# Kernel optimization log

Measured on AMD Instinct MI355X. Metric: run time of the kernel, lower is better.

The kernel has to match this reference:

```python
import jax, jax.numpy as jnp
import numpy as np
import math

BATCH, SEQ, HIDDEN, HEADS = 2, 2048, 1024, 16
HEAD_SIZE = HIDDEN // HEADS
NEG_INF = -10000.0  # faithful to the torch module's masking constant


def setup_inputs() -> dict:
    key = jax.random.key(0)
    k1, k2, k3, k4 = jax.random.split(key, 4)
    x = jax.random.normal(k1, (BATCH, SEQ, HIDDEN), dtype=jnp.float32)
    pos_table = jax.random.normal(k2, (SEQ, HIDDEN), dtype=jnp.float32) * 0.02
    # torch nn.Linear weight layout: [out_features, in_features]
    Wqkv = jax.random.normal(k3, (3 * HIDDEN, HIDDEN), dtype=jnp.float32) * (1.0 / math.sqrt(HIDDEN))
    Wout = jax.random.normal(k4, (HIDDEN, HIDDEN), dtype=jnp.float32) * (1.0 / math.sqrt(HIDDEN))
    return {"x": x, "pos_table": pos_table, "Wqkv": Wqkv, "Wout": Wout}


def reference(x, pos_table, Wqkv, Wout):
    b, n, h = x.shape
    # positional embedding added for Q/K projection only (V uses raw x)
    xp = x + pos_table[None, :n, :]
    qk = jnp.einsum('bnd,ed->bne', xp, Wqkv[: 2 * HIDDEN])          # [b, n, 2h]
    q, k = jnp.split(qk, 2, axis=-1)
    v = jnp.einsum('bnd,ed->bne', x, Wqkv[2 * HIDDEN:])             # [b, n, h]

    def to_heads(t):  # b n (h l) -> b h n l
        return t.reshape(b, n, HEADS, HEAD_SIZE).transpose(0, 2, 1, 3)

    q, k, v = to_heads(q), to_heads(k), to_heads(v)

    scores = jnp.einsum('bhql,bhkl->bhqk', q, k) / math.sqrt(HEAD_SIZE)
    q_ind = jnp.arange(n)[:, None]
    k_ind = jnp.arange(n)[None, :]
    mask = q_ind < k_ind                                            # True where future
    scores = jnp.where(mask, NEG_INF, scores)
    probs = jax.nn.softmax(scores, axis=-1)
    combined_v = jnp.einsum('bhqk,bhkl->bhql', probs, v)            # [b, h, n, l]
    combined_v = combined_v.transpose(0, 2, 1, 3).reshape(b, n, h)  # b h q l -> b q (h l)
    out = jnp.einsum('bnd,ed->bne', combined_v, Wout)
    return out
```

## Files before the change

### kernel.cpp

```cpp
#include <hip/hip_runtime.h>
#include <hip/hip_bf16.h>
#include <stdint.h>

#define BATCH 2
#define SEQ   2048
#define HID   1024
#define NHEAD 16
#define HD    64
#define MROWS (BATCH*SEQ)

typedef __attribute__((ext_vector_type(8))) short bf16x8;
typedef __attribute__((ext_vector_type(4))) float f32x4;

__device__ inline unsigned pk2(float a, float b){
  __hip_bfloat162 h = __float22bfloat162_rn(make_float2(a, b));
  union { __hip_bfloat162 h; unsigned u; } v; v.h = h;
  return v.u;
}
__device__ inline float fexp2(float x){
#if __has_builtin(__builtin_amdgcn_exp2f)
  return __builtin_amdgcn_exp2f(x);
#else
  return exp2f(x);
#endif
}
__device__ inline void lds_load16(const short* g, short* l){
  __builtin_amdgcn_global_load_lds(
      (const __attribute__((address_space(1))) void*)g,
      (__attribute__((address_space(3))) void*)l, 16, 0, 0);
}

__global__ __launch_bounds__(256) void cast_xpos(
    const float* __restrict__ x, const float* __restrict__ pos,
    short* __restrict__ xb, short* __restrict__ xv){
  int i = blockIdx.x * 256 + threadIdx.x;
  float4 xa = ((const float4*)x)[i];
  float4 pa = ((const float4*)pos)[i & (SEQ*HID/4 - 1)];
  uint2 sb, sv;
  sb.x = pk2(xa.x + pa.x, xa.y + pa.y);
  sb.y = pk2(xa.z + pa.z, xa.w + pa.w);
  sv.x = pk2(xa.x, xa.y);
  sv.y = pk2(xa.z, xa.w);
  ((uint2*)xb)[i] = sb;
  ((uint2*)xv)[i] = sv;
}

__global__ __launch_bounds__(256) void cast_w2(
    const float* __restrict__ w1, const float* __restrict__ w2,
    short* __restrict__ o1, short* __restrict__ o2){
  int i = blockIdx.x * 256 + threadIdx.x;
  const int n1 = 3*HID*HID/4;
  const float4* src; uint2* dst; int j;
  if (i < n1){ src = (const float4*)w1; dst = (uint2*)o1; j = i; }
  else       { src = (const float4*)w2; dst = (uint2*)o2; j = i - n1; }
  float4 a = src[j];
  uint2 s;
  s.x = pk2(a.x, a.y);
  s.y = pk2(a.z, a.w);
  dst[j] = s;
}

template<bool F32OUT>
__global__ __launch_bounds__(256) void gemm_bt(
    const short* __restrict__ A0, const short* __restrict__ A1, int split_bx,
    const short* __restrict__ W, void* __restrict__ Cout, int K, int ldc,
    int qsb, float qscale){
  __shared__ alignas(16) short As[2][128*32];
  __shared__ alignas(16) short Bs[2][128*32];
  const int bx = blockIdx.x, by = blockIdx.y;
  const short* A = (bx < split_bx) ? A0 : A1;
  const int tid  = threadIdx.x;
  const int w    = tid >> 6, lane = tid & 63;
  const int g    = lane >> 4, c = lane & 15;
  const int wr   = w >> 1, wc = w & 1;

  f32x4 acc[4][4];
#pragma unroll
  for (int m = 0; m < 4; ++m)
#pragma unroll
    for (int n = 0; n < 4; ++n) acc[m][n] = (f32x4){0.f, 0.f, 0.f, 0.f};

  const short* Abase = A + (size_t)(by*128) * K;
  const short* Wbase = W + (size_t)(bx*128) * K;

  auto stage = [&](int buf, int kt){
#pragma unroll
    for (int j = 0; j < 2; ++j){
      int ci  = w*128 + j*64 + lane;
      int row = ci >> 2, sub = ci & 3;
      lds_load16(Abase + (size_t)row*K + kt + sub*8, &As[buf][(w*128 + j*64)*8]);
      lds_load16(Wbase + (size_t)row*K + kt + sub*8, &Bs[buf][(w*128 + j*64)*8]);
    }
  };

  const int nk = K >> 5;
  stage(0, 0);
  int buf = 0;
  for (int ki = 0; ki < nk; ++ki){
    __syncthreads();
    if (ki + 1 < nk) stage(buf ^ 1, (ki + 1) * 32);

    bf16x8 af[4], bfr[4];
#pragma unroll
    for (int m = 0; m < 4; ++m)
      af[m] = *(const bf16x8*)&As[buf][(wr*64 + m*16 + c)*32 + g*8];
#pragma unroll
    for (int n = 0; n < 4; ++n)
      bfr[n] = *(const bf16x8*)&Bs[buf][(wc*64 + n*16 + c)*32 + g*8];
    __builtin_amdgcn_s_setprio(1);
#pragma unroll
    for (int m = 0; m < 4; ++m)
#pragma unroll
      for (int n = 0; n < 4; ++n)
        acc[m][n] = __builtin_amdgcn_mfma_f32_16x16x32_bf16(af[m], bfr[n], acc[m][n], 0, 0, 0);
    __builtin_amdgcn_s_setprio(0);
    buf ^= 1;
  }

  const float sc = (bx < qsb) ? qscale : 1.0f;
  const int row0 = by*128 + wr*64;
  const int col0 = bx*128 + wc*64;
#pragma unroll
  for (int m = 0; m < 4; ++m)
#pragma unroll
    for (int n = 0; n < 4; ++n){
      size_t base = (size_t)(row0 + m*16 + g*4) * ldc + (col0 + n*16 + c);
      if constexpr (F32OUT){
#pragma unroll
        for (int r = 0; r < 4; ++r)
          ((float*)Cout)[base + (size_t)r*ldc] = acc[m][n][r] * sc;
      } else {
        short* p = (short*)Cout + base;
        unsigned u01 = pk2(acc[m][n][0]*sc, acc[m][n][1]*sc);
        unsigned u23 = pk2(acc[m][n][2]*sc, acc[m][n][3]*sc);
        p[0]             = (short)(u01 & 0xffff);
        p[(size_t)ldc]   = (short)(u01 >> 16);
        p[2*(size_t)ldc] = (short)(u23 & 0xffff);
        p[3*(size_t)ldc] = (short)(u23 >> 16);
      }
    }
}

__global__ __launch_bounds__(256) void attn_fwd(
    const short* __restrict__ qkv, short* __restrict__ out){
  const int bid = blockIdx.x;
  const int qt  = 31 - (bid >> 5);
  const int bh  = bid & 31;
  const int b   = bh >> 4, h = bh & 15;
  const int tid = threadIdx.x;
  const int w   = tid >> 6, lane = tid & 63;
  const int g   = lane >> 4, c = lane & 15;

  __shared__ alignas(16) short Ks[2][64*64];
  __shared__ alignas(16) short Vt[2][64*64];

  const int q0 = qt*64 + w*16;
  const size_t rowb = (size_t)b * SEQ;

  const short* qptr = qkv + (rowb + q0 + c)*3072 + h*HD;
  bf16x8 qf0 = *(const bf16x8*)(qptr + g*8);
  bf16x8 qf1 = *(const bf16x8*)(qptr + 32 + g*8);

  const short* kbase = qkv + rowb*3072 + HID   + h*HD;
  const short* vbase = qkv + rowb*3072 + 2*HID + h*HD;

  const int slot   = ((lane >> 5) << 5) | (((lane >> 2) & 3) << 3)
                   | (((lane >> 4) & 1) << 2) | (lane & 3);
  const int vchunk = slot >> 3, vcol = slot & 7;

  auto stageK = [&](int buf, int c0){
#pragma unroll
    for (int j = 0; j < 2; ++j){
      int pc  = w*128 + j*64 + lane;
      int row = pc >> 3;
      int lc  = (pc & 7) ^ (row & 7);
      lds_load16(kbase + (size_t)(c0 + row)*3072 + lc*8, &Ks[buf][(w*128 + j*64)*8]);
    }
  };
  auto loadV = [&](int c0, bf16x8& v0, bf16x8& v1){
    const short* vp = vbase + (size_t)(c0 + lane)*3072 + w*16;
    v0 = *(const bf16x8*)(vp);
    v1 = *(const bf16x8*)(vp + 8);
  };
  auto scatterV = [&](int buf, const bf16x8& v0, const bf16x8& v1){
#pragma unroll
    for (int j = 0; j < 8; ++j)
      Vt[buf][(w*16 + j)*64 + ((vchunk ^ (j & 7)) << 3) + vcol] = v0[j];
#pragma unroll
    for (int j = 0; j < 8; ++j)
      Vt[buf][(w*16 + 8 + j)*64 + ((vchunk ^ ((8 + j) & 7)) << 3) + vcol] = v1[j];
  };

  f32x4 ot[4];
#pragma unroll
  for (int dt = 0; dt < 4; ++dt) ot[dt] = (f32x4){0.f, 0.f, 0.f, 0.f};
  float mrow = -1e30f, lrow = 0.f;
  const int qg = q0 + c;

  {
    bf16x8 v0, v1;
    stageK(0, 0);
    loadV(0, v0, v1);
    scatterV(0, v0, v1);
  }
  int cur = 0;
  for (int ch = 0; ch <= qt; ++ch){
    const int c0 = ch * 64;
    __syncthreads();

    bf16x8 nv0, nv1;
    if (ch < qt){
      stageK(cur ^ 1, c0 + 64);
      loadV(c0 + 64, nv0, nv1);
    }

    f32x4 s[4];
    __builtin_amdgcn_s_setprio(1);
#pragma unroll
    for (int kt = 0; kt < 4; ++kt){
      int row = kt*16 + c;
      bf16x8 k0 = *(const bf16x8*)&Ks[cur][row*64 + ((g       ^ (row&7))<<3)];
      bf16x8 k1 = *(const bf16x8*)&Ks[cur][row*64 + (((4 + g) ^ (row&7))<<3)];
      f32x4 z = (f32x4){0.f, 0.f, 0.f, 0.f};
      s[kt] = __builtin_amdgcn_mfma_f32_16x16x32_bf16(k0, qf0, z, 0, 0, 0);
      s[kt] = __builtin_amdgcn_mfma_f32_16x16x32_bf16(k1, qf1, s[kt], 0, 0, 0);
    }
    __builtin_amdgcn_s_setprio(0);

    float pv[16];
#pragma unroll
    for (int kt = 0; kt < 4; ++kt)
#pragma unroll
      for (int r = 0; r < 4; ++r) pv[kt*4 + r] = s[kt][r];

    if (ch == qt){
#pragma unroll
      for (int kt = 0; kt < 4; ++kt)
#pragma unroll
        for (int r = 0; r < 4; ++r){
          int ki = c0 + kt*16 + g*4 + r;
          if (ki > qg) pv[kt*4 + r] = -1e30f;
        }
    }

    float a0 = fmaxf(fmaxf(pv[0],  pv[1]),  pv[2]);
    float a1 = fmaxf(fmaxf(pv[3],  pv[4]),  pv[5]);
    float a2 = fmaxf(fmaxf(pv[6],  pv[7]),  pv[8]);
    float a3 = fmaxf(fmaxf(pv[9],  pv[10]), pv[11]);
    float a4 = fmaxf(fmaxf(pv[12], pv[13]), pv[14]);
    float cm = fmaxf(fmaxf(fmaxf(a0, a1), a2), fmaxf(fmaxf(a3, a4), pv[15]));
    cm = fmaxf(cm, __shfl_xor(cm, 16));
    cm = fmaxf(cm, __shfl_xor(cm, 32));
    if (__any(cm > mrow + 8.0f)){
      float mnew  = fmaxf(mrow, cm);
      float alpha = fexp2(mrow - mnew);
      lrow *= alpha;
#pragma unroll
      for (int dt = 0; dt < 4; ++dt)
#pragma unroll
        for (int r = 0; r < 4; ++r) ot[dt][r] *= alpha;
      mrow = mnew;
    }
    float ps = 0.f;
#pragma unroll
    for (int i = 0; i < 16; ++i){ pv[i] = fexp2(pv[i] - mrow); ps += pv[i]; }
    ps += __shfl_xor(ps, 16);
    ps += __shfl_xor(ps, 32);
    lrow += ps;

    union { unsigned u[4]; bf16x8 v; } pb0, pb1;
    pb0.u[0] = pk2(pv[0],  pv[1]);  pb0.u[1] = pk2(pv[2],  pv[3]);
    pb0.u[2] = pk2(pv[4],  pv[5]);  pb0.u[3] = pk2(pv[6],  pv[7]);
    pb1.u[0] = pk2(pv[8],  pv[9]);  pb1.u[1] = pk2(pv[10], pv[11]);
    pb1.u[2] = pk2(pv[12], pv[13]); pb1.u[3] = pk2(pv[14], pv[15]);

    __builtin_amdgcn_s_setprio(1);
#pragma unroll
    for (int dt = 0; dt < 4; ++dt){
      int d = dt*16 + c;
      bf16x8 va0 = *(const bf16x8*)&Vt[cur][d*64 + ((g       ^ (d&7))<<3)];
      bf16x8 va1 = *(const bf16x8*)&Vt[cur][d*64 + (((4 + g) ^ (d&7))<<3)];
      ot[dt] = __builtin_amdgcn_mfma_f32_16x16x32_bf16(va0, pb0.v, ot[dt], 0, 0, 0);
      ot[dt] = __builtin_amdgcn_mfma_f32_16x16x32_bf16(va1, pb1.v, ot[dt], 0, 0, 0);
    }
    __builtin_amdgcn_s_setprio(0);

    if (ch < qt) scatterV(cur ^ 1, nv0, nv1);
    cur ^= 1;
  }

  float inv = 1.f / lrow;
  short* obase = out + (rowb + q0 + c)*HID + h*HD + g*4;
#pragma unroll
  for (int dt = 0; dt < 4; ++dt){
    uint2 uu;
    uu.x = pk2(ot[dt][0]*inv, ot[dt][1]*inv);
    uu.y = pk2(ot[dt][2]*inv, ot[dt][3]*inv);
    *(uint2*)(obase + dt*16) = uu;
  }
}

extern "C" void kernel_launch(void* const* d_in, const int* in_sizes, int n_in,
                              void* d_out, int out_size, void* d_ws, size_t ws_size,
                              hipStream_t stream){
  const float* x    = (const float*)d_in[0];
  const float* pos  = (const float*)d_in[1];
  const float* Wqkv = (const float*)d_in[2];
  const float* Wout = (const float*)d_in[3];

  short* xb     = (short*)d_ws;
  short* xv     = xb    + (size_t)MROWS*HID;
  short* wqkvb  = xv    + (size_t)MROWS*HID;
  short* woutb  = wqkvb + (size_t)3*HID*HID;
  short* qkv    = woutb + (size_t)HID*HID;
  short* attn_o = xb;

  cast_xpos<<<dim3(MROWS*HID/1024), 256, 0, stream>>>(x, pos, xb, xv);
  cast_w2<<<dim3(4*HID*HID/1024), 256, 0, stream>>>(Wqkv, Wout, wqkvb, woutb);

  gemm_bt<false><<<dim3(24, 32), 256, 0, stream>>>(xb, xv, 16, wqkvb, qkv, HID, 3*HID,
                                                   8, 0.18033688011112042f);

  attn_fwd<<<dim3(1024), 256, 0, stream>>>(qkv, attn_o);

  gemm_bt<true><<<dim3(8, 32), 256, 0, stream>>>(attn_o, attn_o, 8, woutb, d_out, HID, HID,
                                                 0, 1.0f);
}
```

Baseline: 197.1 us.

## Process 128 query rows per attention block to double K/V tile reuse

Each attention block now handles a 128-row query tile, with every wave owning two 16-row query groups (A and B) that share each staged K/V chunk from LDS. This halves the K/V global loads and LDS staging per query and halves the grid to 512 blocks. Waves skip chunks that lie entirely beyond their causal range. The cost is twice the accumulator and softmax registers per wave, which may lower occupancy. Causal work is also less balanced, since waves in the same block idle on the last chunks and there are fewer blocks to spread over the CUs.

```diff
diff --git a/kernel.cpp b/kernel.cpp
--- a/kernel.cpp
+++ b/kernel.cpp
@@ -144,7 +144,7 @@
 __global__ __launch_bounds__(256) void attn_fwd(
     const short* __restrict__ qkv, short* __restrict__ out){
   const int bid = blockIdx.x;
-  const int qt  = 31 - (bid >> 5);
+  const int qt  = 15 - (bid >> 5);
   const int bh  = bid & 31;
   const int b   = bh >> 4, h = bh & 15;
   const int tid = threadIdx.x;
@@ -154,12 +154,15 @@
   __shared__ alignas(16) short Ks[2][64*64];
   __shared__ alignas(16) short Vt[2][64*64];
 
-  const int q0 = qt*64 + w*16;
+  const int q0 = qt*128 + w*32;
   const size_t rowb = (size_t)b * SEQ;
 
-  const short* qptr = qkv + (rowb + q0 + c)*3072 + h*HD;
-  bf16x8 qf0 = *(const bf16x8*)(qptr + g*8);
-  bf16x8 qf1 = *(const bf16x8*)(qptr + 32 + g*8);
+  const short* qptrA = qkv + (rowb + q0 + c)*3072 + h*HD;
+  const short* qptrB = qptrA + 16*3072;
+  bf16x8 qfA0 = *(const bf16x8*)(qptrA + g*8);
+  bf16x8 qfA1 = *(const bf16x8*)(qptrA + 32 + g*8);
+  bf16x8 qfB0 = *(const bf16x8*)(qptrB + g*8);
+  bf16x8 qfB1 = *(const bf16x8*)(qptrB + 32 + g*8);
 
   const short* kbase = qkv + rowb*3072 + HID   + h*HD;
   const short* vbase = qkv + rowb*3072 + 2*HID + h*HD;
@@ -191,11 +194,14 @@
       Vt[buf][(w*16 + 8 + j)*64 + ((vchunk ^ ((8 + j) & 7)) << 3) + vcol] = v1[j];
   };
 
-  f32x4 ot[4];
-#pragma unroll
-  for (int dt = 0; dt < 4; ++dt) ot[dt] = (f32x4){0.f, 0.f, 0.f, 0.f};
-  float mrow = -1e30f, lrow = 0.f;
-  const int qg = q0 + c;
+  f32x4 otA[4], otB[4];
+#pragma unroll
+  for (int dt = 0; dt < 4; ++dt){
+    otA[dt] = (f32x4){0.f, 0.f, 0.f, 0.f};
+    otB[dt] = (f32x4){0.f, 0.f, 0.f, 0.f};
+  }
+  float mA = -1e30f, lA = 0.f, mB = -1e30f, lB = 0.f;
+  const int qgA = q0 + c, qgB = q0 + 16 + c;
 
   {
     bf16x8 v0, v1;
@@ -204,99 +210,135 @@
     scatterV(0, v0, v1);
   }
   int cur = 0;
-  for (int ch = 0; ch <= qt; ++ch){
+  const int nch = 2*qt + 2;
+  for (int ch = 0; ch < nch; ++ch){
     const int c0 = ch * 64;
     __syncthreads();
 
     bf16x8 nv0, nv1;
-    if (ch < qt){
+    if (ch + 1 < nch){
       stageK(cur ^ 1, c0 + 64);
       loadV(c0 + 64, nv0, nv1);
     }
 
-    f32x4 s[4];
-    __builtin_amdgcn_s_setprio(1);
-#pragma unroll
-    for (int kt = 0; kt < 4; ++kt){
-      int row = kt*16 + c;
-      bf16x8 k0 = *(const bf16x8*)&Ks[cur][row*64 + ((g       ^ (row&7))<<3)];
-      bf16x8 k1 = *(const bf16x8*)&Ks[cur][row*64 + (((4 + g) ^ (row&7))<<3)];
-      f32x4 z = (f32x4){0.f, 0.f, 0.f, 0.f};
-      s[kt] = __builtin_amdgcn_mfma_f32_16x16x32_bf16(k0, qf0, z, 0, 0, 0);
-      s[kt] = __builtin_amdgcn_mfma_f32_16x16x32_bf16(k1, qf1, s[kt], 0, 0, 0);
-    }
-    __builtin_amdgcn_s_setprio(0);
-
-    float pv[16];
-#pragma unroll
-    for (int kt = 0; kt < 4; ++kt)
-#pragma unroll
-      for (int r = 0; r < 4; ++r) pv[kt*4 + r] = s[kt][r];
-
-    if (ch == qt){
+    if (c0 <= q0 + 31){
+      f32x4 sA[4], sB[4];
+      __builtin_amdgcn_s_setprio(1);
+#pragma unroll
+      for (int kt = 0; kt < 4; ++kt){
+        int row = kt*16 + c;
+        bf16x8 k0 = *(const bf16x8*)&Ks[cur][row*64 + ((g       ^ (row&7))<<3)];
+        bf16x8 k1 = *(const bf16x8*)&Ks[cur][row*64 + (((4 + g) ^ (row&7))<<3)];
+        f32x4 z = (f32x4){0.f, 0.f, 0.f, 0.f};
+        sA[kt] = __builtin_amdgcn_mfma_f32_16x16x32_bf16(k0, qfA0, z, 0, 0, 0);
+        sA[kt] = __builtin_amdgcn_mfma_f32_16x16x32_bf16(k1, qfA1, sA[kt], 0, 0, 0);
+        sB[kt] = __builtin_amdgcn_mfma_f32_16x16x32_bf16(k0, qfB0, z, 0, 0, 0);
+        sB[kt] = __builtin_amdgcn_mfma_f32_16x16x32_bf16(k1, qfB1, sB[kt], 0, 0, 0);
+      }
+      __builtin_amdgcn_s_setprio(0);
+
+      float pa[16], pb[16];
 #pragma unroll
       for (int kt = 0; kt < 4; ++kt)
 #pragma unroll
         for (int r = 0; r < 4; ++r){
-          int ki = c0 + kt*16 + g*4 + r;
-          if (ki > qg) pv[kt*4 + r] = -1e30f;
+          pa[kt*4 + r] = sA[kt][r];
+          pb[kt*4 + r] = sB[kt][r];
         }
-    }
-
-    float a0 = fmaxf(fmaxf(pv[0],  pv[1]),  pv[2]);
-    float a1 = fmaxf(fmaxf(pv[3],  pv[4]),  pv[5]);
-    float a2 = fmaxf(fmaxf(pv[6],  pv[7]),  pv[8]);
-    float a3 = fmaxf(fmaxf(pv[9],  pv[10]), pv[11]);
-    float a4 = fmaxf(fmaxf(pv[12], pv[13]), pv[14]);
-    float cm = fmaxf(fmaxf(fmaxf(a0, a1), a2), fmaxf(fmaxf(a3, a4), pv[15]));
-    cm = fmaxf(cm, __shfl_xor(cm, 16));
-    cm = fmaxf(cm, __shfl_xor(cm, 32));
-    if (__any(cm > mrow + 8.0f)){
-      float mnew  = fmaxf(mrow, cm);
-      float alpha = fexp2(mrow - mnew);
-      lrow *= alpha;
-#pragma unroll
-      for (int dt = 0; dt < 4; ++dt)
-#pragma unroll
-        for (int r = 0; r < 4; ++r) ot[dt][r] *= alpha;
-      mrow = mnew;
-    }
-    float ps = 0.f;
-#pragma unroll
-    for (int i = 0; i < 16; ++i){ pv[i] = fexp2(pv[i] - mrow); ps += pv[i]; }
-    ps += __shfl_xor(ps, 16);
-    ps += __shfl_xor(ps, 32);
-    lrow += ps;
-
-    union { unsigned u[4]; bf16x8 v; } pb0, pb1;
-    pb0.u[0] = pk2(pv[0],  pv[1]);  pb0.u[1] = pk2(pv[2],  pv[3]);
-    pb0.u[2] = pk2(pv[4],  pv[5]);  pb0.u[3] = pk2(pv[6],  pv[7]);
-    pb1.u[0] = pk2(pv[8],  pv[9]);  pb1.u[1] = pk2(pv[10], pv[11]);
-    pb1.u[2] = pk2(pv[12], pv[13]); pb1.u[3] = pk2(pv[14], pv[15]);
-
-    __builtin_amdgcn_s_setprio(1);
-#pragma unroll
-    for (int dt = 0; dt < 4; ++dt){
-      int d = dt*16 + c;
-      bf16x8 va0 = *(const bf16x8*)&Vt[cur][d*64 + ((g       ^ (d&7))<<3)];
-      bf16x8 va1 = *(const bf16x8*)&Vt[cur][d*64 + (((4 + g) ^ (d&7))<<3)];
-      ot[dt] = __builtin_amdgcn_mfma_f32_16x16x32_bf16(va0, pb0.v, ot[dt], 0, 0, 0);
-      ot[dt] = __builtin_amdgcn_mfma_f32_16x16x32_bf16(va1, pb1.v, ot[dt], 0, 0, 0);
-    }
-    __builtin_amdgcn_s_setprio(0);
-
-    if (ch < qt) scatterV(cur ^ 1, nv0, nv1);
+
+      if (ch >= nch - 2){
+#pragma unroll
+        for (int kt = 0; kt < 4; ++kt)
+#pragma unroll
+          for (int r = 0; r < 4; ++r){
+            int ki = c0 + kt*16 + g*4 + r;
+            if (ki > qgA) pa[kt*4 + r] = -1e30f;
+            if (ki > qgB) pb[kt*4 + r] = -1e30f;
+          }
+      }
+
+      float cmA = fmaxf(fmaxf(fmaxf(pa[0], pa[1]),  fmaxf(pa[2],  pa[3])),
+                        fmaxf(fmaxf(pa[4], pa[5]),  fmaxf(pa[6],  pa[7])));
+      cmA = fmaxf(cmA, fmaxf(fmaxf(fmaxf(pa[8],  pa[9]),  fmaxf(pa[10], pa[11])),
+                             fmaxf(fmaxf(pa[12], pa[13]), fmaxf(pa[14], pa[15]))));
+      float cmB = fmaxf(fmaxf(fmaxf(pb[0], pb[1]),  fmaxf(pb[2],  pb[3])),
+                        fmaxf(fmaxf(pb[4], pb[5]),  fmaxf(pb[6],  pb[7])));
+      cmB = fmaxf(cmB, fmaxf(fmaxf(fmaxf(pb[8],  pb[9]),  fmaxf(pb[10], pb[11])),
+                             fmaxf(fmaxf(pb[12], pb[13]), fmaxf(pb[14], pb[15]))));
+      cmA = fmaxf(cmA, __shfl_xor(cmA, 16));
+      cmA = fmaxf(cmA, __shfl_xor(cmA, 32));
+      cmB = fmaxf(cmB, __shfl_xor(cmB, 16));
+      cmB = fmaxf(cmB, __shfl_xor(cmB, 32));
+      if (__any(cmA > mA + 8.0f)){
+        float mnew  = fmaxf(mA, cmA);
+        float alpha = fexp2(mA - mnew);
+        lA *= alpha;
+#pragma unroll
+        for (int dt = 0; dt < 4; ++dt)
+#pragma unroll
+          for (int r = 0; r < 4; ++r) otA[dt][r] *= alpha;
+        mA = mnew;
+      }
+      if (__any(cmB > mB + 8.0f)){
+        float mnew  = fmaxf(mB, cmB);
+        float alpha = fexp2(mB - mnew);
+        lB *= alpha;
+#pragma unroll
+        for (int dt = 0; dt < 4; ++dt)
+#pragma unroll
+          for (int r = 0; r < 4; ++r) otB[dt][r] *= alpha;
+        mB = mnew;
+      }
+      float psA = 0.f, psB = 0.f;
+#pragma unroll
+      for (int i = 0; i < 16; ++i){
+        pa[i] = fexp2(pa[i] - mA); psA += pa[i];
+        pb[i] = fexp2(pb[i] - mB); psB += pb[i];
+      }
+      psA += __shfl_xor(psA, 16); psA += __shfl_xor(psA, 32);
+      psB += __shfl_xor(psB, 16); psB += __shfl_xor(psB, 32);
+      lA += psA; lB += psB;
+
+      union { unsigned u[4]; bf16x8 v; } pA0, pA1, pB0, pB1;
+      pA0.u[0] = pk2(pa[0],  pa[1]);  pA0.u[1] = pk2(pa[2],  pa[3]);
+      pA0.u[2] = pk2(pa[4],  pa[5]);  pA0.u[3] = pk2(pa[6],  pa[7]);
+      pA1.u[0] = pk2(pa[8],  pa[9]);  pA1.u[1] = pk2(pa[10], pa[11]);
+      pA1.u[2] = pk2(pa[12], pa[13]); pA1.u[3] = pk2(pa[14], pa[15]);
+      pB0.u[0] = pk2(pb[0],  pb[1]);  pB0.u[1] = pk2(pb[2],  pb[3]);
+      pB0.u[2] = pk2(pb[4],  pb[5]);  pB0.u[3] = pk2(pb[6],  pb[7]);
+      pB1.u[0] = pk2(pb[8],  pb[9]);  pB1.u[1] = pk2(pb[10], pb[11]);
+      pB1.u[2] = pk2(pb[12], pb[13]); pB1.u[3] = pk2(pb[14], pb[15]);
+
+      __builtin_amdgcn_s_setprio(1);
+#pragma unroll
+      for (int dt = 0; dt < 4; ++dt){
+        int d = dt*16 + c;
+        bf16x8 va0 = *(const bf16x8*)&Vt[cur][d*64 + ((g       ^ (d&7))<<3)];
+        bf16x8 va1 = *(const bf16x8*)&Vt[cur][d*64 + (((4 + g) ^ (d&7))<<3)];
+        otA[dt] = __builtin_amdgcn_mfma_f32_16x16x32_bf16(va0, pA0.v, otA[dt], 0, 0, 0);
+        otA[dt] = __builtin_amdgcn_mfma_f32_16x16x32_bf16(va1, pA1.v, otA[dt], 0, 0, 0);
+        otB[dt] = __builtin_amdgcn_mfma_f32_16x16x32_bf16(va0, pB0.v, otB[dt], 0, 0, 0);
+        otB[dt] = __builtin_amdgcn_mfma_f32_16x16x32_bf16(va1, pB1.v, otB[dt], 0, 0, 0);
+      }
+      __builtin_amdgcn_s_setprio(0);
+    }
+
+    if (ch + 1 < nch) scatterV(cur ^ 1, nv0, nv1);
     cur ^= 1;
   }
 
-  float inv = 1.f / lrow;
-  short* obase = out + (rowb + q0 + c)*HID + h*HD + g*4;
+  float invA = 1.f / lA, invB = 1.f / lB;
+  short* obA = out + (rowb + q0 + c)*HID + h*HD + g*4;
+  short* obB = obA + 16*HID;
 #pragma unroll
   for (int dt = 0; dt < 4; ++dt){
-    uint2 uu;
-    uu.x = pk2(ot[dt][0]*inv, ot[dt][1]*inv);
-    uu.y = pk2(ot[dt][2]*inv, ot[dt][3]*inv);
-    *(uint2*)(obase + dt*16) = uu;
+    uint2 ua, ub;
+    ua.x = pk2(otA[dt][0]*invA, otA[dt][1]*invA);
+    ua.y = pk2(otA[dt][2]*invA, otA[dt][3]*invA);
+    ub.x = pk2(otB[dt][0]*invB, otB[dt][1]*invB);
+    ub.y = pk2(otB[dt][2]*invB, otB[dt][3]*invB);
+    *(uint2*)(obA + dt*16) = ua;
+    *(uint2*)(obB + dt*16) = ub;
   }
 }
 
@@ -321,7 +363,7 @@
   gemm_bt<false><<<dim3(24, 32), 256, 0, stream>>>(xb, xv, 16, wqkvb, qkv, HID, 3*HID,
                                                    8, 0.18033688011112042f);
 
-  attn_fwd<<<dim3(1024), 256, 0, stream>>>(qkv, attn_o);
+  attn_fwd<<<dim3(512), 256, 0, stream>>>(qkv, attn_o);
 
   gemm_bt<true><<<dim3(8, 32), 256, 0, stream>>>(attn_o, attn_o, 8, woutb, d_out, HID, HID,
                                                  0, 1.0f);
```

After: 213.0 us. 8.1% more time.

## Merge cast kernels and remap GEMM workgroups across XCDs

Applied to the files above, without the earlier changes.

Fuses the activation and weight cast kernels into one launch over a combined index range, removing one kernel launch. The GEMM now uses a 1D grid with a workgroup-ID remap that places contiguous tiles on the same XCD (stride-8 interleave), aiming to improve L2 reuse of A/W tiles on MI355X's multi-die layout. The remap assumes the grid size is divisible by 8, which holds for 768 and 256.

```diff
diff --git a/kernel.cpp b/kernel.cpp
--- a/kernel.cpp
+++ b/kernel.cpp
@@ -30,44 +30,49 @@
       (__attribute__((address_space(3))) void*)l, 16, 0, 0);
 }
 
-__global__ __launch_bounds__(256) void cast_xpos(
+__global__ __launch_bounds__(256) void cast_all(
     const float* __restrict__ x, const float* __restrict__ pos,
-    short* __restrict__ xb, short* __restrict__ xv){
-  int i = blockIdx.x * 256 + threadIdx.x;
-  float4 xa = ((const float4*)x)[i];
-  float4 pa = ((const float4*)pos)[i & (SEQ*HID/4 - 1)];
-  uint2 sb, sv;
-  sb.x = pk2(xa.x + pa.x, xa.y + pa.y);
-  sb.y = pk2(xa.z + pa.z, xa.w + pa.w);
-  sv.x = pk2(xa.x, xa.y);
-  sv.y = pk2(xa.z, xa.w);
-  ((uint2*)xb)[i] = sb;
-  ((uint2*)xv)[i] = sv;
-}
-
-__global__ __launch_bounds__(256) void cast_w2(
     const float* __restrict__ w1, const float* __restrict__ w2,
+    short* __restrict__ xb, short* __restrict__ xv,
     short* __restrict__ o1, short* __restrict__ o2){
   int i = blockIdx.x * 256 + threadIdx.x;
-  const int n1 = 3*HID*HID/4;
-  const float4* src; uint2* dst; int j;
-  if (i < n1){ src = (const float4*)w1; dst = (uint2*)o1; j = i; }
-  else       { src = (const float4*)w2; dst = (uint2*)o2; j = i - n1; }
-  float4 a = src[j];
-  uint2 s;
-  s.x = pk2(a.x, a.y);
-  s.y = pk2(a.z, a.w);
-  dst[j] = s;
+  const int n0 = MROWS*HID/4;
+  if (i < n0){
+    float4 xa = ((const float4*)x)[i];
+    float4 pa = ((const float4*)pos)[i & (SEQ*HID/4 - 1)];
+    uint2 sb, sv;
+    sb.x = pk2(xa.x + pa.x, xa.y + pa.y);
+    sb.y = pk2(xa.z + pa.z, xa.w + pa.w);
+    sv.x = pk2(xa.x, xa.y);
+    sv.y = pk2(xa.z, xa.w);
+    ((uint2*)xb)[i] = sb;
+    ((uint2*)xv)[i] = sv;
+  } else {
+    int j = i - n0;
+    const int n1 = 3*HID*HID/4;
+    const float4* src; uint2* dst; int k;
+    if (j < n1){ src = (const float4*)w1; dst = (uint2*)o1; k = j; }
+    else       { src = (const float4*)w2; dst = (uint2*)o2; k = j - n1; }
+    float4 a = src[k];
+    uint2 s;
+    s.x = pk2(a.x, a.y);
+    s.y = pk2(a.z, a.w);
+    dst[k] = s;
+  }
 }
 
 template<bool F32OUT>
 __global__ __launch_bounds__(256) void gemm_bt(
     const short* __restrict__ A0, const short* __restrict__ A1, int split_bx,
     const short* __restrict__ W, void* __restrict__ Cout, int K, int ldc,
-    int qsb, float qscale){
+    int gx, int qsb, float qscale){
+  const int nwg  = gridDim.x;
+  const int q    = nwg >> 3;
+  const int wgid = (blockIdx.x % 8) * q + (blockIdx.x / 8);
+  const int bx = wgid % gx, by = wgid / gx;
+
   __shared__ alignas(16) short As[2][128*32];
   __shared__ alignas(16) short Bs[2][128*32];
-  const int bx = blockIdx.x, by = blockIdx.y;
   const short* A = (bx < split_bx) ? A0 : A1;
   const int tid  = threadIdx.x;
   const int w    = tid >> 6, lane = tid & 63;
@@ -315,14 +320,14 @@
   short* qkv    = woutb + (size_t)HID*HID;
   short* attn_o = xb;
 
-  cast_xpos<<<dim3(MROWS*HID/1024), 256, 0, stream>>>(x, pos, xb, xv);
-  cast_w2<<<dim3(4*HID*HID/1024), 256, 0, stream>>>(Wqkv, Wout, wqkvb, woutb);
-
-  gemm_bt<false><<<dim3(24, 32), 256, 0, stream>>>(xb, xv, 16, wqkvb, qkv, HID, 3*HID,
-                                                   8, 0.18033688011112042f);
+  cast_all<<<dim3(8192), 256, 0, stream>>>(x, pos, Wqkv, Wout,
+                                           xb, xv, wqkvb, woutb);
+
+  gemm_bt<false><<<dim3(768), 256, 0, stream>>>(xb, xv, 16, wqkvb, qkv, HID, 3*HID,
+                                                24, 8, 0.18033688011112042f);
 
   attn_fwd<<<dim3(1024), 256, 0, stream>>>(qkv, attn_o);
 
-  gemm_bt<true><<<dim3(8, 32), 256, 0, stream>>>(attn_o, attn_o, 8, woutb, d_out, HID, HID,
-                                                 0, 1.0f);
-}
+  gemm_bt<true><<<dim3(256), 256, 0, stream>>>(attn_o, attn_o, 8, woutb, d_out, HID, HID,
+                                               8, 0, 1.0f);
+}
```

After: 191.1 us. -3.0%, faster.
